# Kernel optimization log

Measured on AMD Instinct MI355X. Metric: run time of the kernel, lower is better.

## Reference

```python
import jax, jax.numpy as jnp
import numpy as np

B, L, E, H = 64, 256, 1024, 16
HD = E // H
ROPE_BASE = 10000.0


def rope(x):
    # x: [B, H, L, HD]; torchtune-style interleaved RoPE along the seq axis
    Lx, D = x.shape[2], x.shape[3]
    inv_freq = 1.0 / (ROPE_BASE ** (jnp.arange(0, D, 2, dtype=jnp.float32) / D))
    ang = jnp.arange(Lx, dtype=jnp.float32)[:, None] * inv_freq[None, :]  # [L, D/2]
    cos, sin = jnp.cos(ang), jnp.sin(ang)
    x0, x1 = x[..., 0::2], x[..., 1::2]
    r0 = x0 * cos - x1 * sin
    r1 = x1 * cos + x0 * sin
    return jnp.stack([r0, r1], axis=-1).reshape(x.shape)


def setup_inputs() -> dict:
    key = jax.random.key(0)
    ks = jax.random.split(key, 6)
    s = 0.02
    return {
        "x": jax.random.normal(ks[0], (B, L, E), jnp.float32),
        "Wq": jax.random.normal(ks[1], (E, E), jnp.float32) * s,
        "bq": jnp.zeros((E,), jnp.float32),
        "Wk": jax.random.normal(ks[2], (E, E), jnp.float32) * s,
        "bk": jnp.zeros((E,), jnp.float32),
        "Wv": jax.random.normal(ks[3], (E, E), jnp.float32) * s,
        "bv": jnp.zeros((E,), jnp.float32),
        "Wo": jax.random.normal(ks[4], (E, E), jnp.float32) * s,
        "bo": jnp.zeros((E,), jnp.float32),
        "attention_mask": jnp.ones((B, L), bool),
    }


def reference(x, Wq, bq, Wk, bk, Wv, bv, Wo, bo, attention_mask):
    Bq, Lq, _ = x.shape
    # QKV projections (nn.Linear: y = x @ W.T + b), split heads -> [B, H, L, HD]
    q = (x @ Wq.T + bq).reshape(Bq, Lq, H, HD).transpose(0, 2, 1, 3)
    k = (x @ Wk.T + bk).reshape(Bq, Lq, H, HD).transpose(0, 2, 1, 3)
    v = (x @ Wv.T + bv).reshape(Bq, Lq, H, HD).transpose(0, 2, 1, 3)
    q = rope(q)
    k = rope(k)
    # combined causal + padding mask: [B, 1, Lq, Lq]
    causal = jnp.tril(jnp.ones((Lq, Lq), bool))
    mask = causal[None, None, :, :] & attention_mask[:, None, None, :]
    scale = 1.0 / np.sqrt(HD).astype(np.float32)
    scores = jnp.einsum('bhqd,bhkd->bhqk', q, k) * scale
    scores = jnp.where(mask, scores, jnp.finfo(scores.dtype).min)
    attn = jax.nn.softmax(scores, axis=-1)
    out = jnp.einsum('bhqk,bhkd->bhqd', attn, v)
    out = out.transpose(0, 2, 1, 3).reshape(Bq, Lq, E)
    return out @ Wo.T + bo
```

## Files before the change

### kernel.cpp

```cpp
#include <hip/hip_runtime.h>
#include <hip/hip_bf16.h>

typedef __attribute__((ext_vector_type(4))) float f32x4;
typedef __attribute__((ext_vector_type(8))) short s16x8;
typedef unsigned short ushort_t;

__device__ __forceinline__ ushort_t f2bf(float f) {
    union { float f; unsigned u; } v; v.f = f;
    unsigned r = v.u + 0x7fffu + ((v.u >> 16) & 1u);
    return (ushort_t)(r >> 16);
}

__device__ __forceinline__ void gload16(const ushort_t* g, ushort_t* l) {
    __builtin_amdgcn_global_load_lds(
        (const __attribute__((address_space(1))) unsigned int*)g,
        (__attribute__((address_space(3))) unsigned int*)l,
        16, 0, 0);
}

#define BAR()  asm volatile("s_barrier" ::: "memory")
#define LGK0() do { asm volatile("s_waitcnt lgkmcnt(0)" ::: "memory"); __builtin_amdgcn_sched_barrier(0); } while (0)
#define VMC(n) asm volatile("s_waitcnt vmcnt(" #n ")" ::: "memory")

__global__ void cvt_bf16(const float* __restrict__ in, ushort_t* __restrict__ out, int n8) {
    int i = blockIdx.x * blockDim.x + threadIdx.x;
    if (i >= n8) return;
    const float4* p = (const float4*)in;
    float4 a = p[2 * i], b = p[2 * i + 1];
    s16x8 v;
    v[0] = (short)f2bf(a.x); v[1] = (short)f2bf(a.y);
    v[2] = (short)f2bf(a.z); v[3] = (short)f2bf(a.w);
    v[4] = (short)f2bf(b.x); v[5] = (short)f2bf(b.y);
    v[6] = (short)f2bf(b.z); v[7] = (short)f2bf(b.w);
    *(s16x8*)(out + (size_t)i * 8) = v;
}

__global__ void rope_tab_k(float* __restrict__ cosT, float* __restrict__ sinT) {
    int i = blockIdx.x * blockDim.x + threadIdx.x;
    int l = i >> 5, fi = i & 31;
    float inv = powf(10000.f, -2.f * (float)fi / 64.f);
    float ang = (float)l * inv;
    cosT[i] = cosf(ang);
    sinT[i] = sinf(ang);
}


__device__ __forceinline__ void stage32(const ushort_t* __restrict__ src,
                                        ushort_t* chunk, int tid, int kk) {
#pragma unroll
    for (int j = 0; j < 2; ++j) {
        int row = (tid >> 2) + j * 128;
        int gslot = (tid & 3) ^ ((row >> 1) & 3);
        gload16(src + (size_t)row * 1024 + kk + gslot * 8,
                chunk + (size_t)tid * 8 + (size_t)j * 4096);
    }
}

__device__ __forceinline__ s16x8 rdA32(const ushort_t* chunk, int wm, int m, int lane) {
    int row = wm * 128 + m * 16 + (lane & 15);
    int slot = (lane >> 4) ^ ((row >> 1) & 3);
    return *(const s16x8*)&chunk[row * 32 + (slot << 3)];
}
__device__ __forceinline__ s16x8 rdB32(const ushort_t* chunk, int wn, int n, int lane) {
    int row = wn * 64 + n * 16 + (lane & 15);
    int slot = (lane >> 4) ^ ((row >> 1) & 3);
    return *(const s16x8*)&chunk[row * 32 + (slot << 3)];
}

template <int MODE>
__global__ __launch_bounds__(512, 2) void gemm256(const ushort_t* __restrict__ A,
                                                  const ushort_t* __restrict__ Wt,
                                                  const float* __restrict__ bz0,
                                                  const float* __restrict__ bz1,
                                                  const float* __restrict__ bz2,
                                                  ushort_t* __restrict__ o0,
                                                  ushort_t* __restrict__ o1,
                                                  ushort_t* __restrict__ o2,
                                                  float* __restrict__ of,
                                                  const float* __restrict__ cosT,
                                                  const float* __restrict__ sinT,
                                                  int ntn) {
    __shared__ ushort_t lds[4][2][8192];

    const int nwg = 64 * ntn;
    const int orig = blockIdx.x;
    const int wg = (orig % 8) * (nwg / 8) + orig / 8;
    const int tn = wg % ntn, tm = wg / ntn;

    const int tid = threadIdx.x, lane = tid & 63, wid = tid >> 6;
    const int wm = wid >> 2, wn = wid & 3;

    f32x4 acc[8][4];
#pragma unroll
    for (int i = 0; i < 8; ++i)
#pragma unroll
        for (int j = 0; j < 4; ++j) acc[i][j] = (f32x4){0.f, 0.f, 0.f, 0.f};

    const ushort_t* Abase = A + (size_t)(tm * 256) * 1024;
    const ushort_t* Bbase = Wt + (size_t)(tn * 256) * 1024;

#pragma unroll
    for (int p = 0; p < 3; ++p) {
        stage32(Abase, &lds[p][0][0], tid, p * 32);
        stage32(Bbase, &lds[p][1][0], tid, p * 32);
    }

#pragma unroll 1
    for (int u = 0; u < 32; ++u) {
        const ushort_t* cA = &lds[u & 3][0][0];
        const ushort_t* cB = &lds[u & 3][1][0];
        ushort_t* sA = &lds[(u + 3) & 3][0][0];
        ushort_t* sB = &lds[(u + 3) & 3][1][0];
        const int kt = (u + 3 < 32 ? u + 3 : 31) * 32;
        s16x8 b_[4], a_[8];

        VMC(8);
        BAR();
        stage32(Abase, sA, tid, kt);
        stage32(Bbase, sB, tid, kt);
#pragma unroll
        for (int n = 0; n < 4; ++n) b_[n] = rdB32(cB, wn, n, lane);
#pragma unroll
        for (int m = 0; m < 8; ++m) a_[m] = rdA32(cA, wm, m, lane);
        LGK0();
        __builtin_amdgcn_s_setprio(1);
#pragma unroll
        for (int m = 0; m < 8; ++m)
#pragma unroll
            for (int n = 0; n < 4; ++n)
                acc[m][n] = __builtin_amdgcn_mfma_f32_16x16x32_bf16(a_[m], b_[n], acc[m][n], 0, 0, 0);
        __builtin_amdgcn_s_setprio(0);
    }
    VMC(0);

    const int rb0 = tm * 256 + wm * 128 + ((lane >> 4) << 2);
    if (MODE == 0) {
        const int zz = (tn * 256) >> 10;
        const float* bias = (zz == 0) ? bz0 : (zz == 1) ? bz1 : bz2;
        ushort_t* outp = (zz == 0) ? o0 : (zz == 1) ? o1 : o2;
        const bool rope = (zz < 2);
        const int cb = (tn & 3) * 256 + wn * 64;
#pragma unroll
        for (int m = 0; m < 8; ++m) {
#pragma unroll
            for (int n = 0; n < 4; ++n) {
                int col = cb + n * 16 + (lane & 15);
                float bv_ = bias[col];
                int rb = rb0 + m * 16;
#pragma unroll
                for (int r = 0; r < 4; ++r) {
                    float v = acc[m][n][r] + bv_;
                    float res;
                    if (rope) {
                        int l = (rb + r) & 255;
                        int fi = (col & 63) >> 1;
                        float c = cosT[l * 32 + fi], s = sinT[l * 32 + fi];
                        float partner = __shfl_xor(v, 1);
                        res = (col & 1) ? (v * c + partner * s) : (v * c - partner * s);
                    } else {
                        res = v;
                    }
                    outp[(size_t)(rb + r) * 1024 + col] = f2bf(res);
                }
            }
        }
    } else {
        const int cb = wn * 64;
        const int cfull = tn * 256 + cb;
#pragma unroll
        for (int m = 0; m < 8; ++m) {
#pragma unroll
            for (int n = 0; n < 4; ++n) {
                int col = cfull + n * 16 + (lane & 15);
                float bv_ = bz0[col];
                int rb = rb0 + m * 16;
#pragma unroll
                for (int r = 0; r < 4; ++r)
                    of[(size_t)(rb + r) * 1024 + col] = acc[m][n][r] + bv_;
            }
        }
    }
}

__global__ __launch_bounds__(512) void attn_kernel(const ushort_t* __restrict__ qb,
                                                   const ushort_t* __restrict__ kb,
                                                   const ushort_t* __restrict__ vb,
                                                   ushort_t* __restrict__ ab) {
    __shared__ ushort_t Ks[256 * 72];
    __shared__ ushort_t Vt[64 * 264];
    __shared__ ushort_t Ps[8][16 * 264];
    const int bh = blockIdx.x, b = bh >> 4, h = bh & 15;
    const int tid = threadIdx.x, lane = tid & 63, wid = tid >> 6;
    const size_t base = (size_t)b * 256 * 1024 + (size_t)h * 64;

#pragma unroll
    for (int it = 0; it < 4; ++it) {
        int c = tid + it * 512;
        int row = c >> 3, seg = c & 7;
        *(s16x8*)&Ks[row * 72 + seg * 8] =
            *(const s16x8*)&kb[base + (size_t)row * 1024 + seg * 8];
    }
#pragma unroll
    for (int it = 0; it < 4; ++it) {
        int c = tid + it * 512;
        int k = c >> 3, seg = c & 7;
        s16x8 v8 = *(const s16x8*)&vb[base + (size_t)k * 1024 + seg * 8];
#pragma unroll
        for (int j = 0; j < 8; ++j)
            Vt[(seg * 8 + j) * 264 + k] = (ushort_t)v8[j];
    }
    __syncthreads();

#pragma unroll
    for (int ch = 0; ch < 2; ++ch) {
        const int q0 = wid * 32 + ch * 16;
        const int ntop = q0 >> 4;
        s16x8 aq0 = *(const s16x8*)&qb[base + (size_t)(q0 + (lane & 15)) * 1024 + ((lane >> 4) << 3)];
        s16x8 aq1 = *(const s16x8*)&qb[base + (size_t)(q0 + (lane & 15)) * 1024 + 32 + ((lane >> 4) << 3)];

        f32x4 sacc[16];
#pragma unroll
        for (int n = 0; n < 16; ++n) sacc[n] = (f32x4){0.f, 0.f, 0.f, 0.f};
#pragma unroll
        for (int n = 0; n < 16; ++n) {
            if (n <= ntop) {
                const int kr = (n * 16 + (lane & 15)) * 72 + ((lane >> 4) << 3);
                s16x8 b0 = *(const s16x8*)&Ks[kr];
                s16x8 b1 = *(const s16x8*)&Ks[kr + 32];
                sacc[n] = __builtin_amdgcn_mfma_f32_16x16x32_bf16(aq0, b0, sacc[n], 0, 0, 0);
                sacc[n] = __builtin_amdgcn_mfma_f32_16x16x32_bf16(aq1, b1, sacc[n], 0, 0, 0);
            }
        }

        float rinv[4];
#pragma unroll
        for (int r = 0; r < 4; ++r) {
            const int row = q0 + ((lane >> 4) << 2) + r;
            float m = -1e30f;
#pragma unroll
            for (int n = 0; n < 16; ++n) {
                int col = n * 16 + (lane & 15);
                float v = (col <= row) ? sacc[n][r] * 0.125f : -1e30f;
                sacc[n][r] = v;
                m = fmaxf(m, v);
            }
            m = fmaxf(m, __shfl_xor(m, 1));
            m = fmaxf(m, __shfl_xor(m, 2));
            m = fmaxf(m, __shfl_xor(m, 4));
            m = fmaxf(m, __shfl_xor(m, 8));
            float sum = 0.f;
#pragma unroll
            for (int n = 0; n < 16; ++n) {
                float p = __expf(sacc[n][r] - m);
                sacc[n][r] = p;
                sum += p;
            }
            sum += __shfl_xor(sum, 1);
            sum += __shfl_xor(sum, 2);
            sum += __shfl_xor(sum, 4);
            sum += __shfl_xor(sum, 8);
            rinv[r] = 1.f / sum;
#pragma unroll
            for (int n = 0; n < 16; ++n)
                Ps[wid][(((lane >> 4) << 2) + r) * 264 + n * 16 + (lane & 15)] = f2bf(sacc[n][r]);
        }
        __syncthreads();

        f32x4 oa[4];
#pragma unroll
        for (int dt = 0; dt < 4; ++dt) oa[dt] = (f32x4){0.f, 0.f, 0.f, 0.f};
        const int kstop = q0 >> 5;
#pragma unroll
        for (int ks = 0; ks < 8; ++ks) {
            if (ks <= kstop) {
                s16x8 pf = *(const s16x8*)&Ps[wid][(lane & 15) * 264 + ks * 32 + ((lane >> 4) << 3)];
#pragma unroll
                for (int dt = 0; dt < 4; ++dt) {
                    s16x8 vf = *(const s16x8*)&Vt[(dt * 16 + (lane & 15)) * 264 + ks * 32 + ((lane >> 4) << 3)];
                    oa[dt] = __builtin_amdgcn_mfma_f32_16x16x32_bf16(pf, vf, oa[dt], 0, 0, 0);
                }
            }
        }
#pragma unroll
        for (int dt = 0; dt < 4; ++dt) {
#pragma unroll
            for (int r = 0; r < 4; ++r) {
                int row = q0 + ((lane >> 4) << 2) + r;
                int col = h * 64 + dt * 16 + (lane & 15);
                ab[(size_t)(b * 256 + row) * 1024 + col] = f2bf(oa[dt][r] * rinv[r]);
            }
        }
        __syncthreads();
    }
}

extern "C" void kernel_launch(void* const* d_in, const int* in_sizes, int n_in,
                              void* d_out, int out_size, void* d_ws, size_t ws_size,
                              hipStream_t stream) {
    (void)in_sizes; (void)n_in; (void)out_size;
    const float* x  = (const float*)d_in[0];
    const float* Wq = (const float*)d_in[1];
    const float* bq = (const float*)d_in[2];
    const float* Wk = (const float*)d_in[3];
    const float* bk = (const float*)d_in[4];
    const float* Wv = (const float*)d_in[5];
    const float* bv = (const float*)d_in[6];
    const float* Wo = (const float*)d_in[7];
    const float* bo = (const float*)d_in[8];
    float* out = (float*)d_out;

    const size_t M = 16384, E = 1024;
    char* ws = (char*)d_ws;
    ushort_t* xb   = (ushort_t*)ws;
    ushort_t* wqkv = xb + M * E;
    ushort_t* wob  = wqkv + 3 * E * E;
    ushort_t* qb   = wob + E * E;
    ushort_t* kb   = qb + M * E;
    ushort_t* vb   = kb + M * E;
    float* cosT    = (float*)(vb + M * E);
    float* sinT    = cosT + 256 * 32;
    ushort_t* ab   = xb;

    size_t need = (4 * M * E + 4 * E * E) * sizeof(ushort_t) + 2 * 256 * 32 * sizeof(float);
    if (ws_size < need) return;

    cvt_bf16<<<8192, 256, 0, stream>>>(x, xb, (int)(M * E / 8));
    cvt_bf16<<<512, 256, 0, stream>>>(Wq, wqkv, (int)(E * E / 8));
    cvt_bf16<<<512, 256, 0, stream>>>(Wk, wqkv + E * E, (int)(E * E / 8));
    cvt_bf16<<<512, 256, 0, stream>>>(Wv, wqkv + 2 * E * E, (int)(E * E / 8));
    cvt_bf16<<<512, 256, 0, stream>>>(Wo, wob, (int)(E * E / 8));
    rope_tab_k<<<32, 256, 0, stream>>>(cosT, sinT);

    gemm256<0><<<768, 512, 0, stream>>>(xb, wqkv, bq, bk, bv, qb, kb, vb, nullptr,
                                        cosT, sinT, 12);
    attn_kernel<<<1024, 512, 0, stream>>>(qb, kb, vb, ab);
    gemm256<1><<<256, 512, 0, stream>>>(ab, wob, bo, nullptr, nullptr,
                                        nullptr, nullptr, nullptr, out, nullptr, nullptr, 4);
}
```

Before: 281.8 us.

## Restructure GEMM mainloop into 8-phase ping-pong with K=64 half-tile staging

Replaces the 4-stage K=32 LDS ring in the 256x256 bf16 GEMM with a double-buffered K=64 scheme. Each A/B tile is split into row halves that are staged separately, and MFMA work is split into eight barrier-delimited phases that interleave LDS reads, global-to-LDS loads and compute. The swizzle changes to an 8-slot XOR pattern for 64-wide rows. It also merges the four weight conversion launches into one 2D-grid kernel. The extra barriers per phase add sync overhead, and the overlap gain depends on the wait counts being correct.

```diff
diff --git a/kernel.cpp b/kernel.cpp
--- a/kernel.cpp
+++ b/kernel.cpp
@@ -35,6 +35,23 @@
     *(s16x8*)(out + (size_t)i * 8) = v;
 }
 
+__global__ void cvt_w4(const float* __restrict__ w0, const float* __restrict__ w1,
+                       const float* __restrict__ w2, const float* __restrict__ w3,
+                       ushort_t* __restrict__ out) {
+    const float* src = (blockIdx.y == 0) ? w0 : (blockIdx.y == 1) ? w1
+                     : (blockIdx.y == 2) ? w2 : w3;
+    ushort_t* dst = out + (size_t)blockIdx.y * 1024 * 1024;
+    int i = blockIdx.x * blockDim.x + threadIdx.x;
+    const float4* p = (const float4*)src;
+    float4 a = p[2 * i], b = p[2 * i + 1];
+    s16x8 v;
+    v[0] = (short)f2bf(a.x); v[1] = (short)f2bf(a.y);
+    v[2] = (short)f2bf(a.z); v[3] = (short)f2bf(a.w);
+    v[4] = (short)f2bf(b.x); v[5] = (short)f2bf(b.y);
+    v[6] = (short)f2bf(b.z); v[7] = (short)f2bf(b.w);
+    *(s16x8*)(dst + (size_t)i * 8) = v;
+}
+
 __global__ void rope_tab_k(float* __restrict__ cosT, float* __restrict__ sinT) {
     int i = blockIdx.x * blockDim.x + threadIdx.x;
     int l = i >> 5, fi = i & 31;
@@ -45,26 +62,26 @@
 }
 
 
-__device__ __forceinline__ void stage32(const ushort_t* __restrict__ src,
-                                        ushort_t* chunk, int tid, int kk) {
+__device__ __forceinline__ void stage_half(const ushort_t* __restrict__ src,
+                                           ushort_t* chunk, int tid) {
 #pragma unroll
     for (int j = 0; j < 2; ++j) {
-        int row = (tid >> 2) + j * 128;
-        int gslot = (tid & 3) ^ ((row >> 1) & 3);
-        gload16(src + (size_t)row * 1024 + kk + gslot * 8,
+        int row = (tid >> 3) + j * 64;
+        int gslot = (tid & 7) ^ (row & 7);
+        gload16(src + (size_t)row * 1024 + gslot * 8,
                 chunk + (size_t)tid * 8 + (size_t)j * 4096);
     }
 }
 
-__device__ __forceinline__ s16x8 rdA32(const ushort_t* chunk, int wm, int m, int lane) {
-    int row = wm * 128 + m * 16 + (lane & 15);
-    int slot = (lane >> 4) ^ ((row >> 1) & 3);
-    return *(const s16x8*)&chunk[row * 32 + (slot << 3)];
-}
-__device__ __forceinline__ s16x8 rdB32(const ushort_t* chunk, int wn, int n, int lane) {
-    int row = wn * 64 + n * 16 + (lane & 15);
-    int slot = (lane >> 4) ^ ((row >> 1) & 3);
-    return *(const s16x8*)&chunk[row * 32 + (slot << 3)];
+__device__ __forceinline__ s16x8 rdA(const ushort_t* chunk, int m, int kh, int lane) {
+    int row = m * 16 + (lane & 15);
+    int slot = (kh * 4 + (lane >> 4)) ^ (row & 7);
+    return *(const s16x8*)&chunk[row * 64 + (slot << 3)];
+}
+__device__ __forceinline__ s16x8 rdB(const ushort_t* chunk, int wn, int n, int kh, int lane) {
+    int row = (wn & 1) * 64 + n * 16 + (lane & 15);
+    int slot = (kh * 4 + (lane >> 4)) ^ (row & 7);
+    return *(const s16x8*)&chunk[row * 64 + (slot << 3)];
 }
 
 template <int MODE>
@@ -80,7 +97,7 @@
                                                   const float* __restrict__ cosT,
                                                   const float* __restrict__ sinT,
                                                   int ntn) {
-    __shared__ ushort_t lds[4][2][8192];
+    __shared__ ushort_t lds[2][2][2][8192];
 
     const int nwg = 64 * ntn;
     const int orig = blockIdx.x;
@@ -99,39 +116,59 @@
     const ushort_t* Abase = A + (size_t)(tm * 256) * 1024;
     const ushort_t* Bbase = Wt + (size_t)(tn * 256) * 1024;
 
-#pragma unroll
-    for (int p = 0; p < 3; ++p) {
-        stage32(Abase, &lds[p][0][0], tid, p * 32);
-        stage32(Bbase, &lds[p][1][0], tid, p * 32);
-    }
+    const ushort_t* cA0 = &lds[0][0][wm][0];
+    const ushort_t* cB0 = &lds[0][1][wn >> 1][0];
+    const ushort_t* cA1 = &lds[1][0][wm][0];
+    const ushort_t* cB1 = &lds[1][1][wn >> 1][0];
+
+#define SHX(tv, buf, mat, half)                                                        \
+    stage_half(((mat) ? Bbase : Abase) + (size_t)(half) * 131072 + (size_t)(tv) * 64,  \
+               &lds[buf][mat][half][0], tid)
+
+#define RDAL(c, kh) do { _Pragma("unroll") for (int m_ = 0; m_ < 4; ++m_) aL[m_] = rdA(c, m_, kh, lane); } while (0)
+#define RDAH(c, kh) do { _Pragma("unroll") for (int m_ = 0; m_ < 4; ++m_) aH[m_] = rdA(c, m_ + 4, kh, lane); } while (0)
+#define RDB(c, kh)  do { _Pragma("unroll") for (int n_ = 0; n_ < 4; ++n_) bb[n_] = rdB(c, wn, n_, kh, lane); } while (0)
+
+#define PH(MB, AF)                                                                     \
+    do {                                                                               \
+        BAR(); LGK0();                                                                 \
+        __builtin_amdgcn_s_setprio(1);                                                 \
+        _Pragma("unroll") for (int m_ = 0; m_ < 4; ++m_)                               \
+        _Pragma("unroll") for (int n_ = 0; n_ < 4; ++n_)                               \
+            acc[(MB) + m_][n_] = __builtin_amdgcn_mfma_f32_16x16x32_bf16(              \
+                AF[m_], bb[n_], acc[(MB) + m_][n_], 0, 0, 0);                          \
+        __builtin_amdgcn_s_setprio(0);                                                 \
+        BAR();                                                                         \
+    } while (0)
+
+    SHX(0, 0, 1, 0); SHX(0, 0, 1, 1); SHX(0, 0, 0, 0); SHX(0, 0, 0, 1);
+    SHX(1, 1, 1, 0);
+    VMC(2);
+    BAR();
 
 #pragma unroll 1
-    for (int u = 0; u < 32; ++u) {
-        const ushort_t* cA = &lds[u & 3][0][0];
-        const ushort_t* cB = &lds[u & 3][1][0];
-        ushort_t* sA = &lds[(u + 3) & 3][0][0];
-        ushort_t* sB = &lds[(u + 3) & 3][1][0];
-        const int kt = (u + 3 < 32 ? u + 3 : 31) * 32;
-        s16x8 b_[4], a_[8];
-
-        VMC(8);
-        BAR();
-        stage32(Abase, sA, tid, kt);
-        stage32(Bbase, sB, tid, kt);
-#pragma unroll
-        for (int n = 0; n < 4; ++n) b_[n] = rdB32(cB, wn, n, lane);
-#pragma unroll
-        for (int m = 0; m < 8; ++m) a_[m] = rdA32(cA, wm, m, lane);
-        LGK0();
-        __builtin_amdgcn_s_setprio(1);
-#pragma unroll
-        for (int m = 0; m < 8; ++m)
-#pragma unroll
-            for (int n = 0; n < 4; ++n)
-                acc[m][n] = __builtin_amdgcn_mfma_f32_16x16x32_bf16(a_[m], b_[n], acc[m][n], 0, 0, 0);
-        __builtin_amdgcn_s_setprio(0);
+    for (int t = 0; t < 8; ++t) {
+        const int u1 = 2 * t + 1;
+        const int u2 = (2 * t + 2 > 15) ? 15 : 2 * t + 2;
+        const int u3 = (2 * t + 3 > 15) ? 15 : 2 * t + 3;
+        s16x8 aL[4], aH[4], bb[4];
+
+        RDAL(cA0, 0); RDB(cB0, 0); SHX(u1, 1, 1, 1);          PH(0, aL);
+        RDAH(cA0, 0);              SHX(u1, 1, 0, 0);          PH(4, aH);
+        RDAL(cA0, 1); RDB(cB0, 1); SHX(u1, 1, 0, 1);          PH(0, aL);
+        RDAH(cA0, 1);              SHX(u2, 0, 1, 0); VMC(2);  PH(4, aH);
+        RDAL(cA1, 0); RDB(cB1, 0); SHX(u2, 0, 1, 1);          PH(0, aL);
+        RDAH(cA1, 0);              SHX(u2, 0, 0, 0);          PH(4, aH);
+        RDAL(cA1, 1); RDB(cB1, 1); SHX(u2, 0, 0, 1);          PH(0, aL);
+        RDAH(cA1, 1);              SHX(u3, 1, 1, 0); VMC(2);  PH(4, aH);
     }
     VMC(0);
+
+#undef SHX
+#undef RDAL
+#undef RDAH
+#undef RDB
+#undef PH
 
     const int rb0 = tm * 256 + wm * 128 + ((lane >> 4) << 2);
     if (MODE == 0) {
@@ -325,10 +362,7 @@
     if (ws_size < need) return;
 
     cvt_bf16<<<8192, 256, 0, stream>>>(x, xb, (int)(M * E / 8));
-    cvt_bf16<<<512, 256, 0, stream>>>(Wq, wqkv, (int)(E * E / 8));
-    cvt_bf16<<<512, 256, 0, stream>>>(Wk, wqkv + E * E, (int)(E * E / 8));
-    cvt_bf16<<<512, 256, 0, stream>>>(Wv, wqkv + 2 * E * E, (int)(E * E / 8));
-    cvt_bf16<<<512, 256, 0, stream>>>(Wo, wob, (int)(E * E / 8));
+    cvt_w4<<<dim3(512, 4), 256, 0, stream>>>(Wq, Wk, Wv, Wo, wqkv);
     rope_tab_k<<<32, 256, 0, stream>>>(cosT, sinT);
 
     gemm256<0><<<768, 512, 0, stream>>>(xb, wqkv, bq, bk, bv, qb, kb, vb, nullptr,
```

Result: faster. 268.7 us (-4.7%).
